# Kernel optimization log

Hardware: AMD Instinct MI355X
Metric: run time of the kernel (lower is better)

The kernel has to match this reference:

```python
import jax, jax.numpy as jnp
import numpy as np

E = 768
H = 8

def setup_inputs() -> dict:
    key = jax.random.key(0)
    ks = jax.random.split(key, 9)
    s = 1.0 / np.sqrt(E)
    x = jax.random.normal(ks[0], (4, 2048, E), dtype=jnp.float32)
    Wq = jax.random.uniform(ks[1], (E, E), jnp.float32, -s, s)
    bq = jax.random.uniform(ks[2], (E,), jnp.float32, -s, s)
    Wk = jax.random.uniform(ks[3], (E, E), jnp.float32, -s, s)
    bk = jax.random.uniform(ks[4], (E,), jnp.float32, -s, s)
    Wv = jax.random.uniform(ks[5], (E, E), jnp.float32, -s, s)
    bv = jax.random.uniform(ks[6], (E,), jnp.float32, -s, s)
    Wo = jax.random.uniform(ks[7], (E, E), jnp.float32, -s, s)
    bo = jax.random.uniform(ks[8], (E,), jnp.float32, -s, s)
    return {"x": x, "Wq": Wq, "bq": bq, "Wk": Wk, "bk": bk, "Wv": Wv, "bv": bv, "Wo": Wo, "bo": bo}

def reference(x, Wq, bq, Wk, bk, Wv, bv, Wo, bo):
    B, N, Emb = x.shape
    d = Emb // H
    # projections (torch Linear: y = x @ W.T + b)
    q = (x @ Wq.T + bq).reshape(B, N, H, d).transpose(0, 2, 1, 3)  # [B,H,N,d]
    k = (x @ Wk.T + bk).reshape(B, N, H, d).transpose(0, 2, 1, 3)
    v = (x @ Wv.T + bv).reshape(B, N, H, d).transpose(0, 2, 1, 3)
    scores = jnp.einsum('bhnd,bhmd->bhnm', q, k) / jnp.sqrt(jnp.float32(d))
    attn = jax.nn.softmax(scores, axis=-1)  # dropout p=0.0 -> identity
    out = jnp.einsum('bhnm,bhmd->bhnd', attn, v)
    out = out.transpose(0, 2, 1, 3).reshape(B, N, Emb)
    return out @ Wo.T + bo
```

## Files before the change

### kernel.cpp

```cpp
#include <hip/hip_runtime.h>


#define E_DIM 768
#define N_HEAD 8
#define D_HEAD 96
#define B_SZ 4
#define N_SEQ 2048
#define BN (B_SZ * N_SEQ)

typedef unsigned short u16;
typedef __attribute__((ext_vector_type(8))) unsigned short u16x8;
typedef __attribute__((ext_vector_type(4))) unsigned short u16x4;
typedef __attribute__((ext_vector_type(8))) short s16x8;
typedef __attribute__((ext_vector_type(4))) float f32x4;

#define SZ_X   ((size_t)BN * E_DIM)
#define SZ_W   ((size_t)E_DIM * E_DIM)
#define SZ_B   ((size_t)E_DIM)
#define N_CONV (SZ_X + 4 * SZ_W + 4 * SZ_B)

__device__ __forceinline__ float bf2f(u16 u) {
    union { unsigned u; float f; } c; c.u = ((unsigned)u) << 16; return c.f;
}
__device__ __forceinline__ u16 f2bf(float f) {
    union { float f; unsigned u; } c; c.f = f;
    unsigned r = c.u + 0x7FFFu + ((c.u >> 16) & 1u);
    return (u16)(r >> 16);
}
__device__ __forceinline__ void gl_lds16(const u16* g, u16* l) {
    __builtin_amdgcn_global_load_lds(
        (const __attribute__((address_space(1))) unsigned int*)g,
        (__attribute__((address_space(3))) unsigned int*)l, 16, 0, 0);
}

__global__ void detect_dtype(const void* __restrict__ x, int* __restrict__ flag) {
    __shared__ int cnt;
    if (threadIdx.x == 0) cnt = 0;
    __syncthreads();
    const u16* p = (const u16*)x;
    u16 u = p[(size_t)threadIdx.x * 2];
    int ef = (u >> 7) & 0xFF;
    int insane = (ef < 96 || ef > 159) ? 1 : 0;
    atomicAdd(&cnt, insane);
    __syncthreads();
    if (threadIdx.x == 0) *flag = (cnt > 128) ? 1 : 0;
}

__global__ __launch_bounds__(256) void convert8(
    const int* __restrict__ flag,
    const void* __restrict__ x,
    const void* __restrict__ wq, const void* __restrict__ wk,
    const void* __restrict__ wv, const void* __restrict__ wo,
    const void* __restrict__ bq, const void* __restrict__ bk,
    const void* __restrict__ bv, const void* __restrict__ bo,
    u16* __restrict__ dst)
{
    size_t i = ((size_t)blockIdx.x * 256 + threadIdx.x) * 8;
    if (i >= N_CONV) return;
    const int f32 = *flag;
    size_t r = i;
    const void* s;
    if (r < SZ_X) { s = x; }
    else { r -= SZ_X;
      if (r < SZ_W) { s = wq; }
      else { r -= SZ_W;
        if (r < SZ_W) { s = wk; }
        else { r -= SZ_W;
          if (r < SZ_W) { s = wv; }
          else { r -= SZ_W;
            if (r < SZ_W) { s = wo; }
            else { r -= SZ_W;
              if (r < SZ_B) { s = bq; }
              else { r -= SZ_B;
                if (r < SZ_B) { s = bk; }
                else { r -= SZ_B;
                  if (r < SZ_B) { s = bv; }
                  else { r -= SZ_B; s = bo; }
                }
              }
            }
          }
        }
      }
    }
    u16x8 o;
    if (f32) {
        float4 a = ((const float4*)((const float*)s + r))[0];
        float4 b = ((const float4*)((const float*)s + r))[1];
        o[0] = f2bf(a.x); o[1] = f2bf(a.y); o[2] = f2bf(a.z); o[3] = f2bf(a.w);
        o[4] = f2bf(b.x); o[5] = f2bf(b.y); o[6] = f2bf(b.z); o[7] = f2bf(b.w);
    } else {
        o = *(const u16x8*)((const u16*)s + r);
    }
    *(u16x8*)(dst + i) = o;
}

#define GBK 64
#define GBUF (128 * GBK)

#define GEMM_STAGE(Ab, Wb, kt, As_, Bs_)                                        \
    {                                                                           \
        const int kt_ = (kt);                                                   \
        _Pragma("unroll")                                                       \
        for (int j = 0; j < 4; j++) {                                           \
            int st = wave * 4 + j;                                              \
            int row = st * 8 + (lane >> 3);                                     \
            int cl = (lane & 7) ^ ((lane >> 3) & 7);                            \
            gl_lds16(Ab + (size_t)row * E_DIM + kt_ + cl * 8, (As_) + st * 512);\
            gl_lds16(Wb + (size_t)row * E_DIM + kt_ + cl * 8, (Bs_) + st * 512);\
        }                                                                       \
    }

#define GEMM_COMPUTE(As_, Bs_)                                                  \
    {                                                                           \
        _Pragma("unroll")                                                       \
        for (int s = 0; s < 2; s++) {                                           \
            s16x8 af[4], bf[4];                                                 \
            _Pragma("unroll")                                                   \
            for (int mi = 0; mi < 4; mi++) {                                    \
                int row = wm * 64 + mi * 16 + l16;                              \
                af[mi] = *(const s16x8*)&(As_)[row * GBK + ((s * 4 + q4) ^ (l16 & 7)) * 8]; \
            }                                                                   \
            _Pragma("unroll")                                                   \
            for (int ni = 0; ni < 4; ni++) {                                    \
                int row = wn * 64 + ni * 16 + l16;                              \
                bf[ni] = *(const s16x8*)&(Bs_)[row * GBK + ((s * 4 + q4) ^ (l16 & 7)) * 8]; \
            }                                                                   \
            _Pragma("unroll")                                                   \
            for (int mi = 0; mi < 4; mi++)                                      \
                _Pragma("unroll")                                               \
                for (int ni = 0; ni < 4; ni++)                                  \
                    acc[mi][ni] = __builtin_amdgcn_mfma_f32_16x16x32_bf16(      \
                        af[mi], bf[ni], acc[mi][ni], 0, 0, 0);                  \
        }                                                                       \
    }

#define GEMM_KLOOP_DB(Ab, Wb)                                                   \
    GEMM_STAGE(Ab, Wb, 0, smem, smem + GBUF)                                    \
    for (int it = 0; it < 12; it++) {                                           \
        __syncthreads();                                                        \
        if (it < 11) {                                                          \
            u16* An = smem + ((it + 1) & 1) * 2 * GBUF;                         \
            GEMM_STAGE(Ab, Wb, (it + 1) * GBK, An, An + GBUF)                   \
        }                                                                       \
        u16* Ac = smem + (it & 1) * 2 * GBUF;                                   \
        GEMM_COMPUTE(Ac, Ac + GBUF)                                             \
    }

__global__ __launch_bounds__(256) void gemm_mfma_qkv(
    const u16* __restrict__ A, const u16* __restrict__ W,
    const u16* __restrict__ bias, u16* __restrict__ C, u16* __restrict__ Vt)
{
    __shared__ u16 smem[4 * GBUF];
    const int tid = threadIdx.x;
    const int wave = tid >> 6, lane = tid & 63;
    const int q4 = lane >> 4, l16 = lane & 15;
    const int wm = wave & 1, wn = wave >> 1;
    const int bm = blockIdx.x, bn = blockIdx.y;

    f32x4 acc[4][4];
    #pragma unroll
    for (int i = 0; i < 4; i++)
        #pragma unroll
        for (int j = 0; j < 4; j++) acc[i][j] = (f32x4){0.f, 0.f, 0.f, 0.f};

    const u16* Ab = A + (size_t)(bm * 128) * E_DIM;
    const u16* Wb = W + (size_t)(bn * 128) * E_DIM;
    GEMM_KLOOP_DB(Ab, Wb)

    if (bn < 12) {
        u16* Cb = smem;
        u16* Cw = C + (size_t)(bn / 6) * SZ_X;
        const int nc0 = (bn % 6) * 128;
        const int row = tid >> 3, seg = (tid & 7) * 16;
        #pragma unroll
        for (int mi = 0; mi < 4; mi++) {
            __syncthreads();
            #pragma unroll
            for (int ni = 0; ni < 4; ni++) {
                int n_l = wn * 64 + ni * 16 + l16;
                float bi = bf2f(bias[bn * 128 + n_l]);
                #pragma unroll
                for (int r = 0; r < 4; r++)
                    Cb[(wm * 16 + q4 * 4 + r) * 136 + n_l] = f2bf(acc[mi][ni][r] + bi);
            }
            __syncthreads();
            int mrow = bm * 128 + (row >> 4) * 64 + mi * 16 + (row & 15);
            *(u16x8*)(Cw + (size_t)mrow * E_DIM + nc0 + seg)     = *(const u16x8*)&Cb[row * 136 + seg];
            *(u16x8*)(Cw + (size_t)mrow * E_DIM + nc0 + seg + 8) = *(const u16x8*)&Cb[row * 136 + seg + 8];
        }
    } else {
        u16* Cb = smem;
        const int bnv = bn - 12;
        const int b = bm >> 4;
        const int n_l = tid >> 1, m0 = (tid & 1) * 16;
        const size_t vrow = (size_t)(b * 768 + bnv * 128 + n_l);
        #pragma unroll
        for (int mi = 0; mi < 4; mi++) {
            __syncthreads();
            #pragma unroll
            for (int ni = 0; ni < 4; ni++) {
                int nl = wn * 64 + ni * 16 + l16;
                float bi = bf2f(bias[bn * 128 + nl]);
                #pragma unroll
                for (int r = 0; r < 4; r++)
                    Cb[nl * 40 + wm * 16 + q4 * 4 + r] = f2bf(acc[mi][ni][r] + bi);
            }
            __syncthreads();
            int seq0 = (bm & 15) * 128 + (tid & 1) * 64 + mi * 16;
            *(u16x8*)(Vt + vrow * N_SEQ + seq0)     = *(const u16x8*)&Cb[n_l * 40 + m0];
            *(u16x8*)(Vt + vrow * N_SEQ + seq0 + 8) = *(const u16x8*)&Cb[n_l * 40 + m0 + 8];
        }
    }
}

__global__ __launch_bounds__(256) void gemm_mfma_out(
    const u16* __restrict__ A, const u16* __restrict__ W,
    const u16* __restrict__ bias, void* __restrict__ C,
    const int* __restrict__ flag)
{
    __shared__ u16 smem[4 * GBUF];
    const int tid = threadIdx.x;
    const int wave = tid >> 6, lane = tid & 63;
    const int q4 = lane >> 4, l16 = lane & 15;
    const int wm = wave & 1, wn = wave >> 1;
    const int bm = blockIdx.x, bn = blockIdx.y;

    f32x4 acc[4][4];
    #pragma unroll
    for (int i = 0; i < 4; i++)
        #pragma unroll
        for (int j = 0; j < 4; j++) acc[i][j] = (f32x4){0.f, 0.f, 0.f, 0.f};

    const u16* Ab = A + (size_t)(bm * 128) * E_DIM;
    const u16* Wb = W + (size_t)(bn * 128) * E_DIM;
    GEMM_KLOOP_DB(Ab, Wb)

    float* Cbf = (float*)smem;
    const int f32 = *flag;
    const int row = tid >> 3, seg = (tid & 7) * 16;
    #pragma unroll
    for (int mi = 0; mi < 4; mi++) {
        __syncthreads();
        #pragma unroll
        for (int ni = 0; ni < 4; ni++) {
            int n_l = wn * 64 + ni * 16 + l16;
            float bi = bf2f(bias[bn * 128 + n_l]);
            #pragma unroll
            for (int r = 0; r < 4; r++)
                Cbf[(wm * 16 + q4 * 4 + r) * 132 + n_l] = acc[mi][ni][r] + bi;
        }
        __syncthreads();
        int mrow = bm * 128 + (row >> 4) * 64 + mi * 16 + (row & 15);
        if (f32) {
            #pragma unroll
            for (int c = 0; c < 4; c++)
                *(float4*)((float*)C + (size_t)mrow * E_DIM + bn * 128 + seg + c * 4) =
                    *(const float4*)&Cbf[row * 132 + seg + c * 4];
        } else {
            u16x8 o0, o1;
            #pragma unroll
            for (int c = 0; c < 8; c++) {
                o0[c] = f2bf(Cbf[row * 132 + seg + c]);
                o1[c] = f2bf(Cbf[row * 132 + seg + 8 + c]);
            }
            *(u16x8*)((u16*)C + (size_t)mrow * E_DIM + bn * 128 + seg)     = o0;
            *(u16x8*)((u16*)C + (size_t)mrow * E_DIM + bn * 128 + seg + 8) = o1;
        }
    }
}

#define QT2 128
#define KT 64

#define ATTN_STAGE(kt, bb)                                                       \
    {                                                                            \
        const int kt_ = (kt); const int bb_ = (bb);                              \
        _Pragma("unroll")                                                        \
        for (int ii = 0; ii < 3; ii++) {                                         \
            int st = wave + 8 * ii;                                              \
            if (st < 12) {                                                       \
                int plane = st >> 2, sub = st & 3;                               \
                int cip = sub * 64 + lane;                                       \
                int r = cip >> 2;                                                \
                int cs2 = (cip & 3) ^ ((r >> 1) & 3);                            \
                gl_lds16(K + (size_t)(b * N_SEQ + kt_ + r) * E_DIM + h * D_HEAD + plane * 32 + cs2 * 8, \
                         &Ks[bb_][plane * 2048 + sub * 512]);                    \
            } else {                                                             \
                int j = st - 12;                                                 \
                int plane = j / 6, sub = j - plane * 6;                          \
                int cip = sub * 64 + lane;                                       \
                int r = cip >> 2;                                                \
                int cs2 = (cip & 3) ^ ((r >> 1) & 3);                            \
                gl_lds16(Vt + (size_t)((b * N_HEAD + h) * D_HEAD + r) * N_SEQ + kt_ + plane * 32 + cs2 * 8, \
                         &Vts[bb_][plane * 3072 + sub * 512]);                   \
            }                                                                    \
        }                                                                        \
    }

__global__ __launch_bounds__(512) void attn_mfma2(
    const u16* __restrict__ Q, const u16* __restrict__ K,
    const u16* __restrict__ Vt, u16* __restrict__ O)
{
    __shared__ u16 Ks[2][3 * 64 * 32];
    __shared__ u16 Vts[2][2 * 96 * 32];
    __shared__ u16 Ps[8 * 16 * 64];

    const int tid = threadIdx.x;
    const int wave = tid >> 6, lane = tid & 63;
    const int q4 = lane >> 4, l16 = lane & 15;
    const int swz = (l16 >> 1) & 3;
    const int b = blockIdx.z, h = blockIdx.y, qb = blockIdx.x;

    const float SCL2 = 0.10206207261596577f * 1.4426950408889634f;

    const int qrow = qb * QT2 + wave * 16 + l16;
    const u16* qptr = Q + (size_t)(b * N_SEQ + qrow) * E_DIM + h * D_HEAD;
    s16x8 qf[3];
    #pragma unroll
    for (int ks = 0; ks < 3; ks++) {
        u16x8 raw = *(const u16x8*)(qptr + ks * 32 + q4 * 8);
        #pragma unroll
        for (int j = 0; j < 8; j++)
            qf[ks][j] = (short)f2bf(bf2f(raw[j]) * SCL2);
    }

    f32x4 of[6];
    #pragma unroll
    for (int i = 0; i < 6; i++) of[i] = (f32x4){0.f, 0.f, 0.f, 0.f};
    float l_r[4] = {0.f, 0.f, 0.f, 0.f};

    u16* psw = Ps + wave * 16 * 64;

    ATTN_STAGE(0, 0)
    for (int t = 0; t < N_SEQ / KT; t++) {
        __syncthreads();
        if (t < N_SEQ / KT - 1) ATTN_STAGE((t + 1) * KT, (t + 1) & 1)
        const int cb = t & 1;

        f32x4 sf[4];
        #pragma unroll
        for (int i = 0; i < 4; i++) sf[i] = (f32x4){0.f, 0.f, 0.f, 0.f};
        #pragma unroll
        for (int nt = 0; nt < 4; nt++)
            #pragma unroll
            for (int ks = 0; ks < 3; ks++) {
                s16x8 bfr = *(const s16x8*)&Ks[cb][ks * 2048 + (nt * 16 + l16) * 32 + ((q4 ^ swz) << 3)];
                sf[nt] = __builtin_amdgcn_mfma_f32_16x16x32_bf16(qf[ks], bfr, sf[nt], 0, 0, 0);
            }

        #pragma unroll
        for (int nt = 0; nt < 4; nt++)
            #pragma unroll
            for (int r = 0; r < 4; r++) {
                float pv = exp2f(sf[nt][r]);
                l_r[r] += pv;
                int prow = q4 * 4 + r;
                psw[prow * 64 + (((nt * 2 + (l16 >> 3)) ^ (prow & 7)) << 3) + (l16 & 7)] = f2bf(pv);
            }

        #pragma unroll
        for (int ks2 = 0; ks2 < 2; ks2++) {
            s16x8 afr = *(const s16x8*)&psw[l16 * 64 + (((ks2 * 4 + q4) ^ (l16 & 7)) << 3)];
            #pragma unroll
            for (int nt = 0; nt < 6; nt++) {
                s16x8 bfr = *(const s16x8*)&Vts[cb][ks2 * 3072 + (nt * 16 + l16) * 32 + ((q4 ^ swz) << 3)];
                of[nt] = __builtin_amdgcn_mfma_f32_16x16x32_bf16(afr, bfr, of[nt], 0, 0, 0);
            }
        }
    }

    float linv[4];
    #pragma unroll
    for (int r = 0; r < 4; r++) {
        float l = l_r[r];
        #pragma unroll
        for (int off = 1; off < 16; off <<= 1)
            l += __shfl_xor(l, off, 64);
        linv[r] = 1.0f / l;
    }
    u16* optr = O + (size_t)(b * N_SEQ + qb * QT2 + wave * 16) * E_DIM + h * D_HEAD;
    #pragma unroll
    for (int nt = 0; nt < 6; nt++)
        #pragma unroll
        for (int r = 0; r < 4; r++)
            optr[(size_t)(q4 * 4 + r) * E_DIM + nt * 16 + l16] = f2bf(of[nt][r] * linv[r]);
}

extern "C" void kernel_launch(void* const* d_in, const int* in_sizes, int n_in,
                              void* d_out, int out_size, void* d_ws, size_t ws_size,
                              hipStream_t stream) {
    (void)in_sizes; (void)n_in; (void)out_size; (void)ws_size;
    const void* x  = d_in[0];
    const void* Wq = d_in[1]; const void* bq = d_in[2];
    const void* Wk = d_in[3]; const void* bk = d_in[4];
    const void* Wv = d_in[5]; const void* bv = d_in[6];
    const void* Wo = d_in[7]; const void* bo = d_in[8];

    int* flag = (int*)d_ws;
    u16* base = (u16*)d_ws + 8;
    u16* xb  = base;
    u16* wqb = xb  + SZ_X;
    u16* wob = wqb + 3 * SZ_W;
    u16* bqb = wob + SZ_W;
    u16* bob = bqb + 3 * SZ_B;
    u16* q_ws = bob + SZ_B;
    u16* k_ws = q_ws + SZ_X;
    u16* vt_ws = k_ws + SZ_X;
    u16* o_ws = vt_ws + SZ_X;

    detect_dtype<<<1, 256, 0, stream>>>(x, flag);
    convert8<<<(int)((N_CONV / 8 + 255) / 256), 256, 0, stream>>>(
        flag, x, Wq, Wk, Wv, Wo, bq, bk, bv, bo, base);

    gemm_mfma_qkv<<<dim3(BN / 128, 2304 / 128), 256, 0, stream>>>(
        xb, wqb, bqb, q_ws, vt_ws);

    attn_mfma2<<<dim3(N_SEQ / QT2, N_HEAD, B_SZ), 512, 0, stream>>>(
        q_ws, k_ws, vt_ws, o_ws);

    gemm_mfma_out<<<dim3(BN / 128, E_DIM / 128), 256, 0, stream>>>(
        o_ws, wob, bob, d_out, flag);
}
```

Measured before the change: 245.1 us.

## Give each attention wave two 16-row query tiles to reuse K/V fragments

The attention kernel moves from 8 waves with 16 query rows each to 4 waves with 32 query rows each, so every K and V fragment read from LDS feeds two MFMAs. This halves LDS fragment traffic per MFMA and halves the wave count per block, at the cost of more accumulator registers and possibly lower occupancy. P is now rounded to bf16 with a cheaper round-half-up conversion instead of round-to-nearest-even, a slight precision change.

After: 249.2 us. About the same (+1.7%).

```diff
diff --git a/kernel.cpp b/kernel.cpp
--- a/kernel.cpp
+++ b/kernel.cpp
@@ -26,6 +26,10 @@
     union { float f; unsigned u; } c; c.f = f;
     unsigned r = c.u + 0x7FFFu + ((c.u >> 16) & 1u);
     return (u16)(r >> 16);
+}
+__device__ __forceinline__ u16 f2bf_fast(float f) {
+    union { float f; unsigned u; } c; c.f = f;
+    return (u16)((c.u + 0x8000u) >> 16);
 }
 __device__ __forceinline__ void gl_lds16(const u16* g, u16* l) {
     __builtin_amdgcn_global_load_lds(
@@ -270,15 +274,14 @@
     }
 }
 
-#define QT2 128
 #define KT 64
 
 #define ATTN_STAGE(kt, bb)                                                       \
     {                                                                            \
         const int kt_ = (kt); const int bb_ = (bb);                              \
         _Pragma("unroll")                                                        \
-        for (int ii = 0; ii < 3; ii++) {                                         \
-            int st = wave + 8 * ii;                                              \
+        for (int ii = 0; ii < 6; ii++) {                                         \
+            int st = wave + 4 * ii;                                              \
             if (st < 12) {                                                       \
                 int plane = st >> 2, sub = st & 3;                               \
                 int cip = sub * 64 + lane;                                       \
@@ -298,13 +301,13 @@
         }                                                                        \
     }
 
-__global__ __launch_bounds__(512) void attn_mfma2(
+__global__ __launch_bounds__(256) void attn_mfma3(
     const u16* __restrict__ Q, const u16* __restrict__ K,
     const u16* __restrict__ Vt, u16* __restrict__ O)
 {
     __shared__ u16 Ks[2][3 * 64 * 32];
     __shared__ u16 Vts[2][2 * 96 * 32];
-    __shared__ u16 Ps[8 * 16 * 64];
+    __shared__ u16 Ps[4 * 32 * 64];
 
     const int tid = threadIdx.x;
     const int wave = tid >> 6, lane = tid & 63;
@@ -314,23 +317,28 @@
 
     const float SCL2 = 0.10206207261596577f * 1.4426950408889634f;
 
-    const int qrow = qb * QT2 + wave * 16 + l16;
-    const u16* qptr = Q + (size_t)(b * N_SEQ + qrow) * E_DIM + h * D_HEAD;
-    s16x8 qf[3];
-    #pragma unroll
-    for (int ks = 0; ks < 3; ks++) {
-        u16x8 raw = *(const u16x8*)(qptr + ks * 32 + q4 * 8);
-        #pragma unroll
-        for (int j = 0; j < 8; j++)
-            qf[ks][j] = (short)f2bf(bf2f(raw[j]) * SCL2);
-    }
-
-    f32x4 of[6];
-    #pragma unroll
-    for (int i = 0; i < 6; i++) of[i] = (f32x4){0.f, 0.f, 0.f, 0.f};
-    float l_r[4] = {0.f, 0.f, 0.f, 0.f};
-
-    u16* psw = Ps + wave * 16 * 64;
+    s16x8 qf[2][3];
+    #pragma unroll
+    for (int rs = 0; rs < 2; rs++) {
+        const int qrow = qb * 128 + wave * 32 + rs * 16 + l16;
+        const u16* qptr = Q + (size_t)(b * N_SEQ + qrow) * E_DIM + h * D_HEAD;
+        #pragma unroll
+        for (int ks = 0; ks < 3; ks++) {
+            u16x8 raw = *(const u16x8*)(qptr + ks * 32 + q4 * 8);
+            #pragma unroll
+            for (int j = 0; j < 8; j++)
+                qf[rs][ks][j] = (short)f2bf(bf2f(raw[j]) * SCL2);
+        }
+    }
+
+    f32x4 of[2][6];
+    #pragma unroll
+    for (int rs = 0; rs < 2; rs++)
+        #pragma unroll
+        for (int i = 0; i < 6; i++) of[rs][i] = (f32x4){0.f, 0.f, 0.f, 0.f};
+    float l_r[2][4] = {{0.f, 0.f, 0.f, 0.f}, {0.f, 0.f, 0.f, 0.f}};
+
+    u16* psw = Ps + wave * 32 * 64;
 
     ATTN_STAGE(0, 0)
     for (int t = 0; t < N_SEQ / KT; t++) {
@@ -338,53 +346,67 @@
         if (t < N_SEQ / KT - 1) ATTN_STAGE((t + 1) * KT, (t + 1) & 1)
         const int cb = t & 1;
 
-        f32x4 sf[4];
-        #pragma unroll
-        for (int i = 0; i < 4; i++) sf[i] = (f32x4){0.f, 0.f, 0.f, 0.f};
+        f32x4 sf[2][4];
+        #pragma unroll
+        for (int rs = 0; rs < 2; rs++)
+            #pragma unroll
+            for (int i = 0; i < 4; i++) sf[rs][i] = (f32x4){0.f, 0.f, 0.f, 0.f};
         #pragma unroll
         for (int nt = 0; nt < 4; nt++)
             #pragma unroll
             for (int ks = 0; ks < 3; ks++) {
                 s16x8 bfr = *(const s16x8*)&Ks[cb][ks * 2048 + (nt * 16 + l16) * 32 + ((q4 ^ swz) << 3)];
-                sf[nt] = __builtin_amdgcn_mfma_f32_16x16x32_bf16(qf[ks], bfr, sf[nt], 0, 0, 0);
-            }
-
-        #pragma unroll
-        for (int nt = 0; nt < 4; nt++)
-            #pragma unroll
-            for (int r = 0; r < 4; r++) {
-                float pv = exp2f(sf[nt][r]);
-                l_r[r] += pv;
-                int prow = q4 * 4 + r;
-                psw[prow * 64 + (((nt * 2 + (l16 >> 3)) ^ (prow & 7)) << 3) + (l16 & 7)] = f2bf(pv);
-            }
+                #pragma unroll
+                for (int rs = 0; rs < 2; rs++)
+                    sf[rs][nt] = __builtin_amdgcn_mfma_f32_16x16x32_bf16(qf[rs][ks], bfr, sf[rs][nt], 0, 0, 0);
+            }
+
+        #pragma unroll
+        for (int rs = 0; rs < 2; rs++)
+            #pragma unroll
+            for (int nt = 0; nt < 4; nt++)
+                #pragma unroll
+                for (int r = 0; r < 4; r++) {
+                    float pv = exp2f(sf[rs][nt][r]);
+                    l_r[rs][r] += pv;
+                    int prow = rs * 16 + q4 * 4 + r;
+                    psw[prow * 64 + (((nt * 2 + (l16 >> 3)) ^ (prow & 7)) << 3) + (l16 & 7)] = f2bf_fast(pv);
+                }
 
         #pragma unroll
         for (int ks2 = 0; ks2 < 2; ks2++) {
-            s16x8 afr = *(const s16x8*)&psw[l16 * 64 + (((ks2 * 4 + q4) ^ (l16 & 7)) << 3)];
+            s16x8 afr[2];
+            #pragma unroll
+            for (int rs = 0; rs < 2; rs++)
+                afr[rs] = *(const s16x8*)&psw[(rs * 16 + l16) * 64 + (((ks2 * 4 + q4) ^ (l16 & 7)) << 3)];
             #pragma unroll
             for (int nt = 0; nt < 6; nt++) {
                 s16x8 bfr = *(const s16x8*)&Vts[cb][ks2 * 3072 + (nt * 16 + l16) * 32 + ((q4 ^ swz) << 3)];
-                of[nt] = __builtin_amdgcn_mfma_f32_16x16x32_bf16(afr, bfr, of[nt], 0, 0, 0);
-            }
-        }
-    }
-
-    float linv[4];
-    #pragma unroll
-    for (int r = 0; r < 4; r++) {
-        float l = l_r[r];
-        #pragma unroll
-        for (int off = 1; off < 16; off <<= 1)
-            l += __shfl_xor(l, off, 64);
-        linv[r] = 1.0f / l;
-    }
-    u16* optr = O + (size_t)(b * N_SEQ + qb * QT2 + wave * 16) * E_DIM + h * D_HEAD;
-    #pragma unroll
-    for (int nt = 0; nt < 6; nt++)
-        #pragma unroll
-        for (int r = 0; r < 4; r++)
-            optr[(size_t)(q4 * 4 + r) * E_DIM + nt * 16 + l16] = f2bf(of[nt][r] * linv[r]);
+                #pragma unroll
+                for (int rs = 0; rs < 2; rs++)
+                    of[rs][nt] = __builtin_amdgcn_mfma_f32_16x16x32_bf16(afr[rs], bfr, of[rs][nt], 0, 0, 0);
+            }
+        }
+    }
+
+    #pragma unroll
+    for (int rs = 0; rs < 2; rs++) {
+        float linv[4];
+        #pragma unroll
+        for (int r = 0; r < 4; r++) {
+            float l = l_r[rs][r];
+            #pragma unroll
+            for (int off = 1; off < 16; off <<= 1)
+                l += __shfl_xor(l, off, 64);
+            linv[r] = 1.0f / l;
+        }
+        u16* optr = O + (size_t)(b * N_SEQ + qb * 128 + wave * 32 + rs * 16) * E_DIM + h * D_HEAD;
+        #pragma unroll
+        for (int nt = 0; nt < 6; nt++)
+            #pragma unroll
+            for (int r = 0; r < 4; r++)
+                optr[(size_t)(q4 * 4 + r) * E_DIM + nt * 16 + l16] = f2bf(of[rs][nt][r] * linv[r]);
+    }
 }
 
 extern "C" void kernel_launch(void* const* d_in, const int* in_sizes, int n_in,
@@ -416,7 +438,7 @@
     gemm_mfma_qkv<<<dim3(BN / 128, 2304 / 128), 256, 0, stream>>>(
         xb, wqb, bqb, q_ws, vt_ws);
 
-    attn_mfma2<<<dim3(N_SEQ / QT2, N_HEAD, B_SZ), 512, 0, stream>>>(
+    attn_mfma3<<<dim3(N_SEQ / 128, N_HEAD, B_SZ), 256, 0, stream>>>(
         q_ws, k_ws, vt_ws, o_ws);
 
     gemm_mfma_out<<<dim3(BN / 128, E_DIM / 128), 256, 0, stream>>>(
```
